# Optimization experiments

Measured on AMD Instinct MI355X. Metric: run time of the kernel, lower is better.

Reference implementation:

```python
import jax, jax.numpy as jnp
import numpy as np

B, L, E, H = 2, 2048, 512, 8
D = E // H  # head_dim = 64


def setup_inputs() -> dict:
    key = jax.random.key(0)
    ks = jax.random.split(key, 12)
    s = 0.02
    return {
        "values": jax.random.normal(ks[0], (B, L, E), jnp.float32),
        "keys": jax.random.normal(ks[1], (B, L, E), jnp.float32),
        "query": jax.random.normal(ks[2], (B, L, E), jnp.float32),
        "mask": jax.random.randint(ks[3], (B, 1, L, L), 0, 2, jnp.int32),
        "Wv": jax.random.normal(ks[4], (E, E), jnp.float32) * s,
        "bv": jax.random.normal(ks[5], (E,), jnp.float32) * s,
        "Wk": jax.random.normal(ks[6], (E, E), jnp.float32) * s,
        "bk": jax.random.normal(ks[7], (E,), jnp.float32) * s,
        "Wq": jax.random.normal(ks[8], (E, E), jnp.float32) * s,
        "bq": jax.random.normal(ks[9], (E,), jnp.float32) * s,
        "Wo": jax.random.normal(ks[10], (E, E), jnp.float32) * s,
        "bo": jax.random.normal(ks[11], (E,), jnp.float32) * s,
    }


def reference(values, keys, query, mask, Wv, bv, Wk, bk, Wq, bq, Wo, bo):
    b, lq = query.shape[0], query.shape[1]
    # torch Linear: y = x @ W.T + b
    v = (values @ Wv.T + bv).reshape(b, -1, H, D)
    k = (keys @ Wk.T + bk).reshape(b, -1, H, D)
    q = (query @ Wq.T + bq).reshape(b, lq, H, D)
    energy = jnp.einsum("bqhd,bkhd->bhqk", q, k)  # [B,H,Lq,Lk]
    # mask applied BEFORE the scale, as in the original
    energy = jnp.where(mask == 0, jnp.float32(-1e20), energy)
    # NOTE: scales by sqrt(embed_size), not sqrt(head_dim) (faithful)
    attn = jax.nn.softmax(energy / jnp.sqrt(jnp.float32(E)), axis=3)
    out = jnp.einsum("bhql,blhd->bqhd", attn, v).reshape(b, lq, E)
    return out @ Wo.T + bo
```

## Files before the change

### kernel.cpp

```cpp
#include <hip/hip_runtime.h>
#include <hip/hip_bf16.h>
#include <math.h>

#define BB 2
#define LL 2048
#define EE 512
#define HH 8
#define DD 64
#define MM (BB * LL)
#define LW (LL / 64)

typedef short bf16x8 __attribute__((ext_vector_type(8)));
typedef float f32x4 __attribute__((ext_vector_type(4)));
typedef float f32x16 __attribute__((ext_vector_type(16)));

#define MFMA16(a, b, c) __builtin_amdgcn_mfma_f32_16x16x32_bf16((a), (b), (c), 0, 0, 0)
#define MFMA32(a, b, c) __builtin_amdgcn_mfma_f32_32x32x16_bf16((a), (b), (c), 0, 0, 0)

#if __has_builtin(__builtin_amdgcn_exp2f)
#define EXP2(x) __builtin_amdgcn_exp2f(x)
#else
#define EXP2(x) exp2f(x)
#endif

#define QSCALE 0.0637587146f

__device__ __forceinline__ void gl2lds16(const __hip_bfloat16* g, __hip_bfloat16* l) {
    __builtin_amdgcn_global_load_lds(
        (const __attribute__((address_space(1))) unsigned int*)(g),
        (__attribute__((address_space(3))) unsigned int*)(l),
        16, 0, 0);
}

__device__ __forceinline__ uint4 cvt8_bf16(const float4 a, const float4 b) {
    union { __hip_bfloat16 h[8]; uint4 u; } t;
    t.h[0] = __float2bfloat16(a.x); t.h[1] = __float2bfloat16(a.y);
    t.h[2] = __float2bfloat16(a.z); t.h[3] = __float2bfloat16(a.w);
    t.h[4] = __float2bfloat16(b.x); t.h[5] = __float2bfloat16(b.y);
    t.h[6] = __float2bfloat16(b.z); t.h[7] = __float2bfloat16(b.w);
    return t.u;
}

struct PrepArgs {
    const float* xsrc[3];
    __hip_bfloat16* xdst[3];
    const float* wsrc[4];
    __hip_bfloat16* wdst[4];
    const int* mask;
    unsigned long long* mbits;
};

__global__ __launch_bounds__(256) void prep(PrepArgs a) {
    const int blk = blockIdx.x;
    if (blk < 3072) {
        const int t = blk >> 10;
        const int i = ((blk & 1023) * 256 + threadIdx.x) * 8;
        const float* s = a.xsrc[t] + i;
        float4 f0 = *(const float4*)(s);
        float4 f1 = *(const float4*)(s + 4);
        *(uint4*)(a.xdst[t] + i) = cvt8_bf16(f0, f1);
    } else if (blk < 3584) {
        const int r = blk - 3072;
        const int t = r >> 7;
        const int i = ((r & 127) * 256 + threadIdx.x) * 8;
        const float* s = a.wsrc[t] + i;
        float4 f0 = *(const float4*)(s);
        float4 f1 = *(const float4*)(s + 4);
        *(uint4*)(a.wdst[t] + i) = cvt8_bf16(f0, f1);
    } else {
        const int mb = blk - 3584;
        #pragma unroll
        for (int r = 0; r < 16; ++r) {
            const size_t idx = ((size_t)mb * 16 + r) * 256 + threadIdx.x;
            const int m = a.mask[idx];
            const unsigned long long w = __ballot(m != 0);
            if ((threadIdx.x & 63) == 0) a.mbits[idx >> 6] = w;
        }
    }
}

struct QKVArgs {
    const __hip_bfloat16* X[3];
    const __hip_bfloat16* W[3];
    const float* bias[3];
    __hip_bfloat16* O[3];
};

__global__ __launch_bounds__(256) void gemm_qkv(QKVArgs p) {
    __shared__ __hip_bfloat16 As[2][2][64][32];
    __shared__ __hip_bfloat16 Bs[2][2][128][32];

    const int z = blockIdx.z;
    const __hip_bfloat16* __restrict__ X = p.X[z];
    const __hip_bfloat16* __restrict__ W = p.W[z];
    const float* __restrict__ bias = p.bias[z];
    __hip_bfloat16* __restrict__ O = p.O[z];

    const int tid = threadIdx.x;
    const int wave = tid >> 6, lane = tid & 63;
    const int l15 = lane & 15, quad = lane >> 4;
    const int wn = wave * 32;
    const int m0 = blockIdx.y * 64, n0 = blockIdx.x * 128;

    const int lr = lane >> 2;
    const int lc = (lane & 3) * 8;
    const __hip_bfloat16* Ax = X + (size_t)(m0 + wave * 16 + lr) * EE + lc;
    const __hip_bfloat16* Bx = W + (size_t)(n0 + wave * 32 + lr) * EE + lc;

    f32x4 acc[4][2] = {};

    #define STAGE_G(buf, k0)                                                   \
        gl2lds16(Ax + (k0),           &As[buf][0][wave * 16][0]);              \
        gl2lds16(Ax + (k0) + 32,      &As[buf][1][wave * 16][0]);              \
        gl2lds16(Bx + (k0),           &Bs[buf][0][wave * 32][0]);              \
        gl2lds16(Bx + (k0) + 32,      &Bs[buf][1][wave * 32][0]);              \
        gl2lds16(Bx + (k0) + 16 * EE,      &Bs[buf][0][wave * 32 + 16][0]);    \
        gl2lds16(Bx + (k0) + 16 * EE + 32, &Bs[buf][1][wave * 32 + 16][0]);

    STAGE_G(0, 0);
    __syncthreads();

    for (int kt = 0; kt < 8; ++kt) {
        const int cur = kt & 1;
        if (kt < 7) { STAGE_G(cur ^ 1, (kt + 1) * 64); }

        #pragma unroll
        for (int c = 0; c < 2; ++c) {
            bf16x8 af[4], bf2[2];
            #pragma unroll
            for (int i = 0; i < 4; ++i)
                af[i] = *(const bf16x8*)&As[cur][c][i * 16 + l15][quad * 8];
            #pragma unroll
            for (int j = 0; j < 2; ++j)
                bf2[j] = *(const bf16x8*)&Bs[cur][c][wn + j * 16 + l15][quad * 8];
            #pragma unroll
            for (int i = 0; i < 4; ++i)
                #pragma unroll
                for (int j = 0; j < 2; ++j)
                    acc[i][j] = MFMA16(af[i], bf2[j], acc[i][j]);
        }
        __syncthreads();
    }

    if (z == 2) {
        #pragma unroll
        for (int i = 0; i < 4; ++i)
            #pragma unroll
            for (int j = 0; j < 2; ++j) {
                const int n = n0 + wn + j * 16 + l15;
                const float bv = bias[n];
                const int h = n >> 6, d = n & 63;
                union { __hip_bfloat16 hh[4]; ushort4 v4; } pk;
                #pragma unroll
                for (int reg = 0; reg < 4; ++reg)
                    pk.hh[reg] = __float2bfloat16(acc[i][j][reg] + bv);
                const int m = m0 + i * 16 + quad * 4;
                const int bb = m >> 11, l = m & 2047;
                *(ushort4*)&O[(((size_t)bb * HH + h) * DD + d) * LL + l] = pk.v4;
            }
    } else {
        const float oscale = (z == 0) ? QSCALE : 1.0f;
        #pragma unroll
        for (int i = 0; i < 4; ++i)
            #pragma unroll
            for (int j = 0; j < 2; ++j) {
                const int n = n0 + wn + j * 16 + l15;
                const float bv = bias[n];
                #pragma unroll
                for (int reg = 0; reg < 4; ++reg) {
                    const int m = m0 + i * 16 + quad * 4 + reg;
                    O[(size_t)m * EE + n] = __float2bfloat16((acc[i][j][reg] + bv) * oscale);
                }
            }
    }
}

__global__ __launch_bounds__(256) void gemm_out(
    const __hip_bfloat16* __restrict__ X, const __hip_bfloat16* __restrict__ W,
    const float* __restrict__ bias, float* __restrict__ C) {
    __shared__ __hip_bfloat16 As[2][2][64][32];
    __shared__ __hip_bfloat16 Bs[2][2][128][32];

    const int tid = threadIdx.x;
    const int wave = tid >> 6, lane = tid & 63;
    const int l15 = lane & 15, quad = lane >> 4;
    const int wn = wave * 32;
    const int m0 = blockIdx.y * 64, n0 = blockIdx.x * 128;

    const int lr = lane >> 2;
    const int lc = (lane & 3) * 8;
    const __hip_bfloat16* Ax = X + (size_t)(m0 + wave * 16 + lr) * EE + lc;
    const __hip_bfloat16* Bx = W + (size_t)(n0 + wave * 32 + lr) * EE + lc;

    f32x4 acc[4][2] = {};

    STAGE_G(0, 0);
    __syncthreads();

    for (int kt = 0; kt < 8; ++kt) {
        const int cur = kt & 1;
        if (kt < 7) { STAGE_G(cur ^ 1, (kt + 1) * 64); }

        #pragma unroll
        for (int c = 0; c < 2; ++c) {
            bf16x8 af[4], bf2[2];
            #pragma unroll
            for (int i = 0; i < 4; ++i)
                af[i] = *(const bf16x8*)&As[cur][c][i * 16 + l15][quad * 8];
            #pragma unroll
            for (int j = 0; j < 2; ++j)
                bf2[j] = *(const bf16x8*)&Bs[cur][c][wn + j * 16 + l15][quad * 8];
            #pragma unroll
            for (int i = 0; i < 4; ++i)
                #pragma unroll
                for (int j = 0; j < 2; ++j)
                    acc[i][j] = MFMA16(af[i], bf2[j], acc[i][j]);
        }
        __syncthreads();
    }

    #pragma unroll
    for (int i = 0; i < 4; ++i)
        #pragma unroll
        for (int j = 0; j < 2; ++j) {
            const int n = n0 + wn + j * 16 + l15;
            const float bv = bias[n];
            #pragma unroll
            for (int reg = 0; reg < 4; ++reg) {
                const int m = m0 + i * 16 + quad * 4 + reg;
                C[(size_t)m * EE + n] = acc[i][j][reg] + bv;
            }
        }
}

__global__ __launch_bounds__(128, 2) void attn_mfma(
    const __hip_bfloat16* __restrict__ Qb, const __hip_bfloat16* __restrict__ Kb,
    const __hip_bfloat16* __restrict__ vtg, const unsigned long long* __restrict__ mbits,
    float* __restrict__ Op0, float* __restrict__ Op1, float* __restrict__ lp) {
    __shared__ __hip_bfloat16 Ks[2][64][68];
    __shared__ __hip_bfloat16 Vs[2][64][68];

    const int tid = threadIdx.x;
    const int wave = tid >> 6, lane = tid & 63;
    const int l31 = lane & 31, hi = lane >> 5;
    const int b = blockIdx.z >> 1, sp = blockIdx.z & 1;
    const int h = blockIdx.y;
    const int q0 = blockIdx.x * 64;
    const int qrow = q0 + wave * 32 + l31;

    const int srow = tid >> 1, sc0 = (tid & 1) * 32;
    const int NT = LW / 2;
    const int t0 = sp * NT;

    bf16x8 qf[4];
    {
        const __hip_bfloat16* qr = Qb + ((size_t)b * LL + qrow) * EE + h * DD + hi * 8;
        qf[0] = *(const bf16x8*)(qr);
        qf[1] = *(const bf16x8*)(qr + 16);
        qf[2] = *(const bf16x8*)(qr + 32);
        qf[3] = *(const bf16x8*)(qr + 48);
    }

    const __hip_bfloat16* kbase =
        Kb + ((size_t)b * LL + (size_t)t0 * 64 + srow) * EE + h * DD + sc0;
    const __hip_bfloat16* vbase =
        vtg + (((size_t)b * HH + h) * DD + srow) * LL + (size_t)t0 * 64 + sc0;
    const unsigned long long* mrow = mbits + ((size_t)b * LL + qrow) * LW + t0;

    f32x16 o0 = {}, o1 = {};
    float lrun = 0.f;

    {
        uint4 k0 = *(const uint4*)(kbase);
        uint4 k1 = *(const uint4*)(kbase + 8);
        uint4 k2 = *(const uint4*)(kbase + 16);
        uint4 k3 = *(const uint4*)(kbase + 24);
        uint4 v0 = *(const uint4*)(vbase);
        uint4 v1 = *(const uint4*)(vbase + 8);
        uint4 v2 = *(const uint4*)(vbase + 16);
        uint4 v3 = *(const uint4*)(vbase + 24);
        *(uint4*)&Ks[0][srow][sc0] = k0;
        *(uint4*)&Ks[0][srow][sc0 + 8] = k1;
        *(uint4*)&Ks[0][srow][sc0 + 16] = k2;
        *(uint4*)&Ks[0][srow][sc0 + 24] = k3;
        *(uint4*)&Vs[0][srow][sc0] = v0;
        *(uint4*)&Vs[0][srow][sc0 + 8] = v1;
        *(uint4*)&Vs[0][srow][sc0 + 16] = v2;
        *(uint4*)&Vs[0][srow][sc0 + 24] = v3;
    }
    unsigned long long mw_cur = mrow[0];
    __syncthreads();

    for (int t = 0; t < NT; ++t) {
        const int cur = t & 1, nxt = cur ^ 1;
        const bool more = (t + 1) < NT;

        uint4 kn0, kn1, kn2, kn3, vn0, vn1, vn2, vn3;
        unsigned long long mw_n;
        if (more) {
            const __hip_bfloat16* kp = kbase + (size_t)(t + 1) * 64 * EE;
            const __hip_bfloat16* vp = vbase + (t + 1) * 64;
            kn0 = *(const uint4*)(kp);      kn1 = *(const uint4*)(kp + 8);
            kn2 = *(const uint4*)(kp + 16); kn3 = *(const uint4*)(kp + 24);
            vn0 = *(const uint4*)(vp);      vn1 = *(const uint4*)(vp + 8);
            vn2 = *(const uint4*)(vp + 16); vn3 = *(const uint4*)(vp + 24);
            mw_n = mrow[t + 1];
        }

        f32x16 st0 = {}, st1 = {};
        #pragma unroll
        for (int kk = 0; kk < 4; ++kk) {
            bf16x8 kf0 = *(const bf16x8*)&Ks[cur][l31][kk * 16 + hi * 8];
            bf16x8 kf1 = *(const bf16x8*)&Ks[cur][32 + l31][kk * 16 + hi * 8];
            st0 = MFMA32(kf0, qf[kk], st0);
            st1 = MFMA32(kf1, qf[kk], st1);
        }

        const unsigned long long msh = mw_cur >> (4 * hi);
        const unsigned int m32a = (unsigned int)msh;
        const unsigned int m32b = (unsigned int)(msh >> 32);
        bf16x8 pa[4];
        #pragma unroll
        for (int kt = 0; kt < 2; ++kt) {
            const f32x16 stv = kt ? st1 : st0;
            const unsigned int mm = kt ? m32b : m32a;
            float p[16];
            #pragma unroll
            for (int r = 0; r < 16; ++r) {
                const int bit = (r & 3) + 8 * (r >> 2);
                const float e = EXP2(stv[r]);
                p[r] = ((mm >> bit) & 1u) ? e : 0.f;
            }
            lrun += (((p[0] + p[1]) + (p[2] + p[3])) + ((p[4] + p[5]) + (p[6] + p[7])))
                  + (((p[8] + p[9]) + (p[10] + p[11])) + ((p[12] + p[13]) + (p[14] + p[15])));
            unsigned int w[8];
            #pragma unroll
            for (int i = 0; i < 8; ++i) {
                union { __hip_bfloat162 h2; unsigned int u; } cv;
                cv.h2 = __float22bfloat162_rn(make_float2(p[2 * i], p[2 * i + 1]));
                w[i] = cv.u;
            }
            asm volatile("v_permlane32_swap_b32 %0, %1" : "+v"(w[0]), "+v"(w[2]));
            asm volatile("v_permlane32_swap_b32 %0, %1" : "+v"(w[1]), "+v"(w[3]));
            asm volatile("v_permlane32_swap_b32 %0, %1" : "+v"(w[4]), "+v"(w[6]));
            asm volatile("v_permlane32_swap_b32 %0, %1" : "+v"(w[5]), "+v"(w[7]));
            union { unsigned int u[4]; bf16x8 v; } f0, f1;
            f0.u[0] = w[0]; f0.u[1] = w[1]; f0.u[2] = w[2]; f0.u[3] = w[3];
            f1.u[0] = w[4]; f1.u[1] = w[5]; f1.u[2] = w[6]; f1.u[3] = w[7];
            pa[kt * 2] = f0.v;
            pa[kt * 2 + 1] = f1.v;
        }

        #pragma unroll
        for (int wd = 0; wd < 4; ++wd) {
            bf16x8 vf0 = *(const bf16x8*)&Vs[cur][l31][wd * 16 + hi * 8];
            bf16x8 vf1 = *(const bf16x8*)&Vs[cur][32 + l31][wd * 16 + hi * 8];
            o0 = MFMA32(pa[wd], vf0, o0);
            o1 = MFMA32(pa[wd], vf1, o1);
        }

        if (more) {
            *(uint4*)&Ks[nxt][srow][sc0] = kn0;
            *(uint4*)&Ks[nxt][srow][sc0 + 8] = kn1;
            *(uint4*)&Ks[nxt][srow][sc0 + 16] = kn2;
            *(uint4*)&Ks[nxt][srow][sc0 + 24] = kn3;
            *(uint4*)&Vs[nxt][srow][sc0] = vn0;
            *(uint4*)&Vs[nxt][srow][sc0 + 8] = vn1;
            *(uint4*)&Vs[nxt][srow][sc0 + 16] = vn2;
            *(uint4*)&Vs[nxt][srow][sc0 + 24] = vn3;
            mw_cur = mw_n;
        }
        __syncthreads();
    }

    lrun += __shfl_xor(lrun, 32);
    if (hi == 0)
        lp[(((size_t)sp * BB + b) * HH + h) * LL + qrow] = lrun;

    float* Opart = sp ? Op1 : Op0;
    float* Ob = Opart + ((size_t)b * LL + q0 + wave * 32) * EE + h * DD;
    #pragma unroll
    for (int r = 0; r < 16; ++r) {
        const int qr = (r & 3) + 8 * (r >> 2) + 4 * hi;
        Ob[(size_t)qr * EE + l31] = o0[r];
        Ob[(size_t)qr * EE + 32 + l31] = o1[r];
    }
}

__global__ __launch_bounds__(256) void combine(
    const float* __restrict__ Op0, const float* __restrict__ Op1,
    const float* __restrict__ lp, __hip_bfloat16* __restrict__ aob) {
    const int idx = blockIdx.x * 256 + threadIdx.x;
    const int row = idx >> 6;
    const int c0 = (idx & 63) * 8;
    const int b = row >> 11, q = row & 2047;
    const int h = c0 >> 6;
    const float l0 = lp[((size_t)b * HH + h) * LL + q];
    const float l1 = lp[(((size_t)BB + b) * HH + h) * LL + q];
    const float linv = 1.f / (l0 + l1);
    const float* p0 = Op0 + (size_t)row * EE + c0;
    const float* p1 = Op1 + (size_t)row * EE + c0;
    float4 a0 = *(const float4*)(p0);
    float4 a1 = *(const float4*)(p0 + 4);
    float4 b0 = *(const float4*)(p1);
    float4 b1 = *(const float4*)(p1 + 4);
    union { __hip_bfloat16 hh[8]; uint4 u; } pk;
    pk.hh[0] = __float2bfloat16((a0.x + b0.x) * linv);
    pk.hh[1] = __float2bfloat16((a0.y + b0.y) * linv);
    pk.hh[2] = __float2bfloat16((a0.z + b0.z) * linv);
    pk.hh[3] = __float2bfloat16((a0.w + b0.w) * linv);
    pk.hh[4] = __float2bfloat16((a1.x + b1.x) * linv);
    pk.hh[5] = __float2bfloat16((a1.y + b1.y) * linv);
    pk.hh[6] = __float2bfloat16((a1.z + b1.z) * linv);
    pk.hh[7] = __float2bfloat16((a1.w + b1.w) * linv);
    *(uint4*)&aob[(size_t)row * EE + c0] = pk.u;
}

extern "C" void kernel_launch(void* const* d_in, const int* in_sizes, int n_in,
                              void* d_out, int out_size, void* d_ws, size_t ws_size,
                              hipStream_t stream) {
    const float* values = (const float*)d_in[0];
    const float* keys   = (const float*)d_in[1];
    const float* query  = (const float*)d_in[2];
    const int*   mask   = (const int*)d_in[3];
    const float* Wv = (const float*)d_in[4];
    const float* bv = (const float*)d_in[5];
    const float* Wk = (const float*)d_in[6];
    const float* bk = (const float*)d_in[7];
    const float* Wq = (const float*)d_in[8];
    const float* bq = (const float*)d_in[9];
    const float* Wo = (const float*)d_in[10];
    const float* bo = (const float*)d_in[11];
    float* out = (float*)d_out;

    const size_t XS = (size_t)MM * EE * 2;
    const size_t WS = (size_t)EE * EE * 2;
    const size_t MBSZ = (size_t)BB * LL * LL / 8;
    const size_t OPSZ = (size_t)BB * LL * EE * 4;
    char* w = (char*)d_ws;
    __hip_bfloat16* xq  = (__hip_bfloat16*)(w);
    __hip_bfloat16* xk  = (__hip_bfloat16*)(w + XS);
    __hip_bfloat16* xv  = (__hip_bfloat16*)(w + 2 * XS);
    __hip_bfloat16* qb  = (__hip_bfloat16*)(w + 3 * XS);
    __hip_bfloat16* kb  = (__hip_bfloat16*)(w + 4 * XS);
    __hip_bfloat16* vtg = (__hip_bfloat16*)(w + 5 * XS);
    __hip_bfloat16* aob = (__hip_bfloat16*)(w + 6 * XS);
    __hip_bfloat16* wqb = (__hip_bfloat16*)(w + 7 * XS);
    __hip_bfloat16* wkb = (__hip_bfloat16*)(w + 7 * XS + WS);
    __hip_bfloat16* wvb = (__hip_bfloat16*)(w + 7 * XS + 2 * WS);
    __hip_bfloat16* wob = (__hip_bfloat16*)(w + 7 * XS + 3 * WS);
    unsigned long long* mbits = (unsigned long long*)(w + 7 * XS + 4 * WS);
    float* Op0 = (float*)(w);
    float* Op1 = (float*)(w + 7 * XS + 4 * WS + MBSZ);
    float* lp  = (float*)(w + 7 * XS + 4 * WS + MBSZ + OPSZ);

    PrepArgs pa;
    pa.xsrc[0] = query; pa.xsrc[1] = keys; pa.xsrc[2] = values;
    pa.xdst[0] = xq;    pa.xdst[1] = xk;   pa.xdst[2] = xv;
    pa.wsrc[0] = Wq; pa.wsrc[1] = Wk; pa.wsrc[2] = Wv; pa.wsrc[3] = Wo;
    pa.wdst[0] = wqb; pa.wdst[1] = wkb; pa.wdst[2] = wvb; pa.wdst[3] = wob;
    pa.mask = mask; pa.mbits = mbits;

    QKVArgs qa;
    qa.X[0] = xq;  qa.X[1] = xk;  qa.X[2] = xv;
    qa.W[0] = wqb; qa.W[1] = wkb; qa.W[2] = wvb;
    qa.bias[0] = bq; qa.bias[1] = bk; qa.bias[2] = bv;
    qa.O[0] = qb;  qa.O[1] = kb;  qa.O[2] = vtg;

    prep<<<5632, 256, 0, stream>>>(pa);
    gemm_qkv<<<dim3(EE / 128, MM / 64, 3), 256, 0, stream>>>(qa);
    attn_mfma<<<dim3(LL / 64, HH, BB * 2), 128, 0, stream>>>(qb, kb, vtg, mbits, Op0, Op1, lp);
    combine<<<(MM * EE) / 2048, 256, 0, stream>>>(Op0, Op1, lp, aob);
    gemm_out<<<dim3(EE / 128, MM / 64), 256, 0, stream>>>(aob, wob, bo, out);
}
```

Baseline: 183.7 us.

## Split attention KV range four ways with 256-thread blocks and MFMA priority

The attention kernel now splits the key range into four parts instead of two and uses 4-wave blocks covering 128 query rows, so each K/V tile in LDS is shared by more waves and each thread loads less. s_setprio raises wave priority around the MFMA sections. The combine kernel now sums four partial outputs and row sums, which adds extra fp32 partial-output traffic and a larger workspace.

```diff
diff --git a/kernel.cpp b/kernel.cpp
--- a/kernel.cpp
+++ b/kernel.cpp
@@ -9,6 +9,8 @@
 #define DD 64
 #define MM (BB * LL)
 #define LW (LL / 64)
+#define NSP 4
+#define NT (LW / NSP)
 
 typedef short bf16x8 __attribute__((ext_vector_type(8)));
 typedef float f32x4 __attribute__((ext_vector_type(4)));
@@ -233,23 +235,22 @@
         }
 }
 
-__global__ __launch_bounds__(128, 2) void attn_mfma(
+__global__ __launch_bounds__(256, 4) void attn_mfma(
     const __hip_bfloat16* __restrict__ Qb, const __hip_bfloat16* __restrict__ Kb,
     const __hip_bfloat16* __restrict__ vtg, const unsigned long long* __restrict__ mbits,
-    float* __restrict__ Op0, float* __restrict__ Op1, float* __restrict__ lp) {
+    float* __restrict__ Op, float* __restrict__ lp) {
     __shared__ __hip_bfloat16 Ks[2][64][68];
     __shared__ __hip_bfloat16 Vs[2][64][68];
 
     const int tid = threadIdx.x;
     const int wave = tid >> 6, lane = tid & 63;
     const int l31 = lane & 31, hi = lane >> 5;
-    const int b = blockIdx.z >> 1, sp = blockIdx.z & 1;
+    const int b = blockIdx.z >> 2, sp = blockIdx.z & 3;
     const int h = blockIdx.y;
-    const int q0 = blockIdx.x * 64;
+    const int q0 = blockIdx.x * 128;
     const int qrow = q0 + wave * 32 + l31;
 
-    const int srow = tid >> 1, sc0 = (tid & 1) * 32;
-    const int NT = LW / 2;
+    const int srow = tid >> 2, sc0 = (tid & 3) * 16;
     const int t0 = sp * NT;
 
     bf16x8 qf[4];
@@ -273,20 +274,12 @@
     {
         uint4 k0 = *(const uint4*)(kbase);
         uint4 k1 = *(const uint4*)(kbase + 8);
-        uint4 k2 = *(const uint4*)(kbase + 16);
-        uint4 k3 = *(const uint4*)(kbase + 24);
         uint4 v0 = *(const uint4*)(vbase);
         uint4 v1 = *(const uint4*)(vbase + 8);
-        uint4 v2 = *(const uint4*)(vbase + 16);
-        uint4 v3 = *(const uint4*)(vbase + 24);
         *(uint4*)&Ks[0][srow][sc0] = k0;
         *(uint4*)&Ks[0][srow][sc0 + 8] = k1;
-        *(uint4*)&Ks[0][srow][sc0 + 16] = k2;
-        *(uint4*)&Ks[0][srow][sc0 + 24] = k3;
         *(uint4*)&Vs[0][srow][sc0] = v0;
         *(uint4*)&Vs[0][srow][sc0 + 8] = v1;
-        *(uint4*)&Vs[0][srow][sc0 + 16] = v2;
-        *(uint4*)&Vs[0][srow][sc0 + 24] = v3;
     }
     unsigned long long mw_cur = mrow[0];
     __syncthreads();
@@ -295,19 +288,20 @@
         const int cur = t & 1, nxt = cur ^ 1;
         const bool more = (t + 1) < NT;
 
-        uint4 kn0, kn1, kn2, kn3, vn0, vn1, vn2, vn3;
+        uint4 kn0, kn1, vn0, vn1;
         unsigned long long mw_n;
         if (more) {
             const __hip_bfloat16* kp = kbase + (size_t)(t + 1) * 64 * EE;
             const __hip_bfloat16* vp = vbase + (t + 1) * 64;
-            kn0 = *(const uint4*)(kp);      kn1 = *(const uint4*)(kp + 8);
-            kn2 = *(const uint4*)(kp + 16); kn3 = *(const uint4*)(kp + 24);
-            vn0 = *(const uint4*)(vp);      vn1 = *(const uint4*)(vp + 8);
-            vn2 = *(const uint4*)(vp + 16); vn3 = *(const uint4*)(vp + 24);
+            kn0 = *(const uint4*)(kp);
+            kn1 = *(const uint4*)(kp + 8);
+            vn0 = *(const uint4*)(vp);
+            vn1 = *(const uint4*)(vp + 8);
             mw_n = mrow[t + 1];
         }
 
         f32x16 st0 = {}, st1 = {};
+        __builtin_amdgcn_s_setprio(1);
         #pragma unroll
         for (int kk = 0; kk < 4; ++kk) {
             bf16x8 kf0 = *(const bf16x8*)&Ks[cur][l31][kk * 16 + hi * 8];
@@ -315,6 +309,7 @@
             st0 = MFMA32(kf0, qf[kk], st0);
             st1 = MFMA32(kf1, qf[kk], st1);
         }
+        __builtin_amdgcn_s_setprio(0);
 
         const unsigned long long msh = mw_cur >> (4 * hi);
         const unsigned int m32a = (unsigned int)msh;
@@ -351,6 +346,7 @@
             pa[kt * 2 + 1] = f1.v;
         }
 
+        __builtin_amdgcn_s_setprio(1);
         #pragma unroll
         for (int wd = 0; wd < 4; ++wd) {
             bf16x8 vf0 = *(const bf16x8*)&Vs[cur][l31][wd * 16 + hi * 8];
@@ -358,16 +354,13 @@
             o0 = MFMA32(pa[wd], vf0, o0);
             o1 = MFMA32(pa[wd], vf1, o1);
         }
+        __builtin_amdgcn_s_setprio(0);
 
         if (more) {
             *(uint4*)&Ks[nxt][srow][sc0] = kn0;
             *(uint4*)&Ks[nxt][srow][sc0 + 8] = kn1;
-            *(uint4*)&Ks[nxt][srow][sc0 + 16] = kn2;
-            *(uint4*)&Ks[nxt][srow][sc0 + 24] = kn3;
             *(uint4*)&Vs[nxt][srow][sc0] = vn0;
             *(uint4*)&Vs[nxt][srow][sc0 + 8] = vn1;
-            *(uint4*)&Vs[nxt][srow][sc0 + 16] = vn2;
-            *(uint4*)&Vs[nxt][srow][sc0 + 24] = vn3;
             mw_cur = mw_n;
         }
         __syncthreads();
@@ -377,8 +370,8 @@
     if (hi == 0)
         lp[(((size_t)sp * BB + b) * HH + h) * LL + qrow] = lrun;
 
-    float* Opart = sp ? Op1 : Op0;
-    float* Ob = Opart + ((size_t)b * LL + q0 + wave * 32) * EE + h * DD;
+    float* Ob = Op + (size_t)sp * MM * EE
+              + ((size_t)b * LL + q0 + wave * 32) * EE + h * DD;
     #pragma unroll
     for (int r = 0; r < 16; ++r) {
         const int qr = (r & 3) + 8 * (r >> 2) + 4 * hi;
@@ -388,31 +381,35 @@
 }
 
 __global__ __launch_bounds__(256) void combine(
-    const float* __restrict__ Op0, const float* __restrict__ Op1,
-    const float* __restrict__ lp, __hip_bfloat16* __restrict__ aob) {
+    const float* __restrict__ Op, const float* __restrict__ lp,
+    __hip_bfloat16* __restrict__ aob) {
     const int idx = blockIdx.x * 256 + threadIdx.x;
     const int row = idx >> 6;
     const int c0 = (idx & 63) * 8;
     const int b = row >> 11, q = row & 2047;
     const int h = c0 >> 6;
-    const float l0 = lp[((size_t)b * HH + h) * LL + q];
-    const float l1 = lp[(((size_t)BB + b) * HH + h) * LL + q];
-    const float linv = 1.f / (l0 + l1);
-    const float* p0 = Op0 + (size_t)row * EE + c0;
-    const float* p1 = Op1 + (size_t)row * EE + c0;
-    float4 a0 = *(const float4*)(p0);
-    float4 a1 = *(const float4*)(p0 + 4);
-    float4 b0 = *(const float4*)(p1);
-    float4 b1 = *(const float4*)(p1 + 4);
+    float lsum = 0.f;
+    float4 s0 = make_float4(0.f, 0.f, 0.f, 0.f);
+    float4 s1 = make_float4(0.f, 0.f, 0.f, 0.f);
+    #pragma unroll
+    for (int sp = 0; sp < NSP; ++sp) {
+        lsum += lp[(((size_t)sp * BB + b) * HH + h) * LL + q];
+        const float* p = Op + (size_t)sp * MM * EE + (size_t)row * EE + c0;
+        float4 a0 = *(const float4*)(p);
+        float4 a1 = *(const float4*)(p + 4);
+        s0.x += a0.x; s0.y += a0.y; s0.z += a0.z; s0.w += a0.w;
+        s1.x += a1.x; s1.y += a1.y; s1.z += a1.z; s1.w += a1.w;
+    }
+    const float linv = 1.f / lsum;
     union { __hip_bfloat16 hh[8]; uint4 u; } pk;
-    pk.hh[0] = __float2bfloat16((a0.x + b0.x) * linv);
-    pk.hh[1] = __float2bfloat16((a0.y + b0.y) * linv);
-    pk.hh[2] = __float2bfloat16((a0.z + b0.z) * linv);
-    pk.hh[3] = __float2bfloat16((a0.w + b0.w) * linv);
-    pk.hh[4] = __float2bfloat16((a1.x + b1.x) * linv);
-    pk.hh[5] = __float2bfloat16((a1.y + b1.y) * linv);
-    pk.hh[6] = __float2bfloat16((a1.z + b1.z) * linv);
-    pk.hh[7] = __float2bfloat16((a1.w + b1.w) * linv);
+    pk.hh[0] = __float2bfloat16(s0.x * linv);
+    pk.hh[1] = __float2bfloat16(s0.y * linv);
+    pk.hh[2] = __float2bfloat16(s0.z * linv);
+    pk.hh[3] = __float2bfloat16(s0.w * linv);
+    pk.hh[4] = __float2bfloat16(s1.x * linv);
+    pk.hh[5] = __float2bfloat16(s1.y * linv);
+    pk.hh[6] = __float2bfloat16(s1.z * linv);
+    pk.hh[7] = __float2bfloat16(s1.w * linv);
     *(uint4*)&aob[(size_t)row * EE + c0] = pk.u;
 }
 
@@ -436,7 +433,7 @@
     const size_t XS = (size_t)MM * EE * 2;
     const size_t WS = (size_t)EE * EE * 2;
     const size_t MBSZ = (size_t)BB * LL * LL / 8;
-    const size_t OPSZ = (size_t)BB * LL * EE * 4;
+    const size_t OPSZ = (size_t)MM * EE * 4;
     char* w = (char*)d_ws;
     __hip_bfloat16* xq  = (__hip_bfloat16*)(w);
     __hip_bfloat16* xk  = (__hip_bfloat16*)(w + XS);
@@ -450,9 +447,8 @@
     __hip_bfloat16* wvb = (__hip_bfloat16*)(w + 7 * XS + 2 * WS);
     __hip_bfloat16* wob = (__hip_bfloat16*)(w + 7 * XS + 3 * WS);
     unsigned long long* mbits = (unsigned long long*)(w + 7 * XS + 4 * WS);
-    float* Op0 = (float*)(w);
-    float* Op1 = (float*)(w + 7 * XS + 4 * WS + MBSZ);
-    float* lp  = (float*)(w + 7 * XS + 4 * WS + MBSZ + OPSZ);
+    float* Op = (float*)(w + 7 * XS + 4 * WS + MBSZ);
+    float* lp = (float*)(w + 7 * XS + 4 * WS + MBSZ + NSP * OPSZ);
 
     PrepArgs pa;
     pa.xsrc[0] = query; pa.xsrc[1] = keys; pa.xsrc[2] = values;
@@ -469,7 +465,7 @@
 
     prep<<<5632, 256, 0, stream>>>(pa);
     gemm_qkv<<<dim3(EE / 128, MM / 64, 3), 256, 0, stream>>>(qa);
-    attn_mfma<<<dim3(LL / 64, HH, BB * 2), 128, 0, stream>>>(qb, kb, vtg, mbits, Op0, Op1, lp);
-    combine<<<(MM * EE) / 2048, 256, 0, stream>>>(Op0, Op1, lp, aob);
+    attn_mfma<<<dim3(LL / 128, HH, BB * NSP), 256, 0, stream>>>(qb, kb, vtg, mbits, Op, lp);
+    combine<<<(MM * EE) / 2048, 256, 0, stream>>>(Op, lp, aob);
     gemm_out<<<dim3(EE / 128, MM / 64), 256, 0, stream>>>(aob, wob, bo, out);
 }
```

New measurement: 183.5 us. No clear change (-0.1%).
